# Optimization experiments

Measured on AMD Instinct MI355X. Metric: run time of the kernel, lower is better.

Reference implementation:

```python
import jax, jax.numpy as jnp
import numpy as np
import math
from jax import lax

ROT = math.radians(45.0)   # rotation_range in radians
TR = 1.0                   # translation_range
P = 50                     # n_particles
ITERS = 30                 # n_iterations
SUB = 256                  # fitness_subsample
MU = P // 2
C_SIGMA = 0.3
D_SIGMA = 1.0


def axis_angle_to_R(a):
    # a: [..., 3] -> [..., 3, 3] via Rodrigues' formula
    theta = jnp.linalg.norm(a, axis=-1, keepdims=True)
    axis = a / (theta + 1e-8)
    x, y, z = axis[..., 0], axis[..., 1], axis[..., 2]
    o = jnp.zeros_like(x)
    K = jnp.stack([jnp.stack([o, -z, y], -1),
                   jnp.stack([z, o, -x], -1),
                   jnp.stack([-y, x, o], -1)], -2)
    th = theta[..., None]
    I = jnp.eye(3, dtype=a.dtype)
    return I + jnp.sin(th) * K + (1.0 - jnp.cos(th)) * (K @ K)


def chamfer(x, y):
    # x: [M,S,3], y: [M,T,3] -> [M]; symmetric chamfer on squared NN distances
    d2 = (jnp.sum(x * x, -1)[:, :, None] + jnp.sum(y * y, -1)[:, None, :]
          - 2.0 * jnp.einsum('msd,mtd->mst', x, y))
    return jnp.min(d2, axis=2).mean(axis=1) + jnp.min(d2, axis=1).mean(axis=1)


def evaluate(src, tgt, positions):
    # src [B,S,3], tgt [B,T,3], positions [B,Pn,6] -> fitness [B,Pn]
    B, Pn, _ = positions.shape
    R = axis_angle_to_R(positions[..., :3])            # [B,Pn,3,3]
    t = positions[..., 3:]
    transformed = jnp.einsum('bnj,bpkj->bpnk', src, R) + t[:, :, None, :]
    x = transformed.reshape(B * Pn, -1, 3)
    y = jnp.broadcast_to(tgt[:, None], (B, Pn) + tgt.shape[1:]).reshape(B * Pn, -1, 3)
    return chamfer(x, y).reshape(B, Pn)


def clamp6(v):
    return jnp.concatenate([jnp.clip(v[..., :3], -ROT, ROT),
                            jnp.clip(v[..., 3:], -TR, TR)], axis=-1)


def run_cmaes(source, target, key):
    B, N, _ = source.shape
    M = target.shape[1]
    S = min(SUB, N)
    k1, k2, k3 = jax.random.split(key, 3)
    src = source[:, jax.random.permutation(k1, N)[:S], :] if S < N else source
    tgt = target[:, jax.random.permutation(k2, M)[:S], :] if S < M else target

    mean = jnp.zeros((B, 6), jnp.float32)
    sigma = jnp.concatenate([jnp.full((B, 3), ROT * 0.3, jnp.float32),
                             jnp.full((B, 3), TR * 0.3, jnp.float32)], axis=1)
    w = np.log(MU + 0.5) - np.log(np.arange(1, MU + 1))
    w = jnp.asarray(w / w.sum(), jnp.float32)       # [MU] recombination weights
    gbest_pos = mean
    gbest_fit = jnp.full((B,), jnp.inf, jnp.float32)

    def step(carry, k):
        mean, sigma, gbest_pos, gbest_fit = carry
        z = jax.random.normal(k, (B, P, 6), jnp.float32)
        off = clamp6(mean[:, None] + sigma[:, None] * z)        # [B,P,6]
        fit = evaluate(src, tgt, off)                            # [B,P]
        order = jnp.argsort(fit, axis=1)
        pidx = order[:, :MU]
        pz = jnp.take_along_axis(z, pidx[..., None], axis=1)     # [B,MU,6]
        ppos = jnp.take_along_axis(off, pidx[..., None], axis=1)
        mean_new = jnp.einsum('m,bmd->bd', w, ppos)
        mean_z = jnp.einsum('m,bmd->bd', w, pz)
        s = sigma * jnp.exp(C_SIGMA / D_SIGMA * (jnp.mean(jnp.abs(mean_z), -1, keepdims=True) - 1.0))
        s = jnp.concatenate([jnp.clip(s[:, :3], ROT * 0.01, ROT * 0.5),
                             jnp.clip(s[:, 3:], TR * 0.01, TR * 0.5)], axis=1)
        best_fit = jnp.take_along_axis(fit, order[:, :1], axis=1)[:, 0]
        best_pos = jnp.take_along_axis(off, order[:, :1, None], axis=1)[:, 0]
        impr = best_fit < gbest_fit
        gbest_pos = jnp.where(impr[:, None], best_pos, gbest_pos)
        gbest_fit = jnp.where(impr, best_fit, gbest_fit)
        return (mean_new, s, gbest_pos, gbest_fit), None

    keys = jax.random.split(k3, ITERS)
    (mean, sigma, gbest_pos, gbest_fit), _ = lax.scan(step, (mean, sigma, gbest_pos, gbest_fit), keys)

    mean_fit = evaluate(src, tgt, mean[:, None, :])[:, 0]
    gbest_pos = jnp.where((mean_fit < gbest_fit)[:, None], mean, gbest_pos)
    return gbest_pos


def _forward(source, target):
    # Optimization runs under no_grad in the original -> stop_gradient here
    gbest = lax.stop_gradient(run_cmaes(source, target, jax.random.key(42)))
    R = axis_angle_to_R(gbest[:, :3])          # [B,3,3]
    t = gbest[:, 3:]                            # [B,3]
    aligned = jnp.einsum('bnj,bkj->bnk', source, R) + t[:, None, :]
    return R, t, aligned


def setup_inputs() -> dict:
    key = jax.random.key(0)
    k1, k2 = jax.random.split(key)
    source = jax.random.normal(k1, (32, 16384, 3), jnp.float32)
    target = jax.random.normal(k2, (32, 16384, 3), jnp.float32)
    return {"source": source, "target": target}


def reference(source, target):
    return _forward(source, target)
```

## Files before the change

### kernel.cpp

```cpp
#include <hip/hip_runtime.h>
#include <stdint.h>
#include <math.h>

#define NB 32
#define NPTS 16384
#define SS 256
#define POPP 50
#define MUU 25
#define NITERS 30

#define ROTF  ((float)0.7853981633974483)
#define SIG0R ((float)(0.7853981633974483*0.3))
#define SIG0T ((float)0.3)
#define SLOR  ((float)(0.7853981633974483*0.01))
#define SHIR  ((float)(0.7853981633974483*0.5))
#define SLOT  ((float)0.01)
#define SHIT  ((float)0.5)
#define SQRT2F ((float)1.4142135623730951)
#define ULOW  (-0.99999994f)

__host__ __device__ inline uint32_t rotl32(uint32_t v, int n){ return (v<<n)|(v>>(32-n)); }

__host__ __device__ inline void tf2x32(uint32_t k0, uint32_t k1, uint32_t x0, uint32_t x1,
                                       uint32_t &o0, uint32_t &o1){
  uint32_t ks2 = k0 ^ k1 ^ 0x1BD11BDAu;
  x0 += k0; x1 += k1;
#define TFR(r) { x0 += x1; x1 = rotl32(x1, r); x1 ^= x0; }
  TFR(13) TFR(15) TFR(26) TFR(6)
  x0 += k1; x1 += ks2 + 1u;
  TFR(17) TFR(29) TFR(16) TFR(24)
  x0 += ks2; x1 += k0 + 2u;
  TFR(13) TFR(15) TFR(26) TFR(6)
  x0 += k0; x1 += k1 + 3u;
  TFR(17) TFR(29) TFR(16) TFR(24)
  x0 += k1; x1 += ks2 + 4u;
  TFR(13) TFR(15) TFR(26) TFR(6)
  x0 += ks2; x1 += k0 + 5u;
#undef TFR
  o0 = x0; o1 = x1;
}

__device__ inline float erfinv32(float x){
  float w = -log1pf(-x*x);
  float p;
  if (w < 5.0f) {
    w = w - 2.5f;
    p = 2.81022636e-08f;
    p = fmaf(p, w, 3.43273939e-07f);
    p = fmaf(p, w, -3.5233877e-06f);
    p = fmaf(p, w, -4.39150654e-06f);
    p = fmaf(p, w, 0.00021858087f);
    p = fmaf(p, w, -0.00125372503f);
    p = fmaf(p, w, -0.00417768164f);
    p = fmaf(p, w, 0.246640727f);
    p = fmaf(p, w, 1.50140941f);
  } else {
    w = sqrtf(w) - 3.0f;
    p = -0.000200214257f;
    p = fmaf(p, w, 0.000100950558f);
    p = fmaf(p, w, 0.00134934322f);
    p = fmaf(p, w, -0.00367342844f);
    p = fmaf(p, w, 0.00573950773f);
    p = fmaf(p, w, -0.0076224613f);
    p = fmaf(p, w, 0.00943887047f);
    p = fmaf(p, w, 1.00167406f);
    p = fmaf(p, w, 2.83297682f);
  }
  return p * x;
}

__device__ inline void axisangle_R(float ax, float ay, float az, float R[9]){
  float th = sqrtf(ax*ax + ay*ay + az*az);
  float den = th + 1e-8f;
  float ux = ax/den, uy = ay/den, uz = az/den;
  float s = sinf(th), c = cosf(th);
  float omc = 1.0f - c;
  float xx=ux*ux, yy=uy*uy, zz=uz*uz;
  float xy=ux*uy, xz=ux*uz, yz=uy*uz;
  R[0] = 1.0f + omc*(-(yy+zz));
  R[1] = s*(-uz) + omc*xy;
  R[2] = s*uy    + omc*xz;
  R[3] = s*uz    + omc*xy;
  R[4] = 1.0f + omc*(-(xx+zz));
  R[5] = s*(-ux) + omc*yz;
  R[6] = s*(-uy) + omc*xz;
  R[7] = s*ux    + omc*yz;
  R[8] = 1.0f + omc*(-(xx+yy));
}

struct WArr { float w[MUU]; };

__global__ void k_init(float* mean, float* sigma, float* gbest_pos, float* gbest_fit){
  int i = blockIdx.x*blockDim.x + threadIdx.x;
  if (i < NB*6){
    mean[i] = 0.0f;
    gbest_pos[i] = 0.0f;
    int d = i % 6;
    sigma[i] = (d < 3) ? SIG0R : SIG0T;
  }
  if (i < NB) gbest_fit[i] = INFINITY;
}

__global__ void k_genperm(uint64_t* comp, uint32_t sa0, uint32_t sa1,
                          uint32_t sb0, uint32_t sb1, int round){
  int i = blockIdx.x*blockDim.x + threadIdx.x;
  if (i >= 2*NPTS) return;
  int a = i >> 14;
  int idx = i & (NPTS-1);
  uint32_t kk0 = a ? sb0 : sa0;
  uint32_t kk1 = a ? sb1 : sa1;
  uint32_t o0,o1; tf2x32(kk0, kk1, 0u, (uint32_t)idx, o0, o1);
  uint32_t key = o0 ^ o1;
  uint64_t val = (round == 0) ? (uint64_t)idx : (comp[i] & 0x3FFFull);
  comp[i] = ((uint64_t)key << 28) | ((uint64_t)idx << 14) | val;
}

__global__ __launch_bounds__(1024) void k_sort_local(uint64_t* comp){
  __shared__ uint64_t buf[4096];
  int c = blockIdx.x;
  int base = c * 4096;
  int abase = (c & 3) * 4096;
  for (int t = threadIdx.x; t < 4096; t += 1024) buf[t] = comp[base + t];
  __syncthreads();
  for (int k = 2; k <= 4096; k <<= 1){
    for (int j = k >> 1; j > 0; j >>= 1){
      for (int idx = threadIdx.x; idx < 2048; idx += 1024){
        int i = ((idx & ~(j-1)) << 1) | (idx & (j-1));
        int pi = i | j;
        bool dir = (((abase + i) & k) == 0);
        uint64_t A = buf[i], Bv = buf[pi];
        bool sw = dir ? (A > Bv) : (A < Bv);
        if (sw){ buf[i] = Bv; buf[pi] = A; }
      }
      __syncthreads();
    }
  }
  for (int t = threadIdx.x; t < 4096; t += 1024) comp[base + t] = buf[t];
}

__global__ void k_sort_global(uint64_t* comp, int k, int j){
  int t = blockIdx.x*blockDim.x + threadIdx.x;
  if (t >= NPTS) return;
  int a = t >> 13;
  int idx = t & 8191;
  int i = ((idx & ~(j-1)) << 1) | (idx & (j-1));
  int pi = i | j;
  bool dir = ((i & k) == 0);
  uint64_t* arr = comp + (size_t)a * NPTS;
  uint64_t A = arr[i], Bv = arr[pi];
  bool sw = dir ? (A > Bv) : (A < Bv);
  if (sw){ arr[i] = Bv; arr[pi] = A; }
}

__global__ __launch_bounds__(1024) void k_sort_finish(uint64_t* comp, int k){
  __shared__ uint64_t buf[4096];
  int c = blockIdx.x;
  int base = c * 4096;
  int abase = (c & 3) * 4096;
  for (int t = threadIdx.x; t < 4096; t += 1024) buf[t] = comp[base + t];
  __syncthreads();
  for (int j = 2048; j > 0; j >>= 1){
    for (int idx = threadIdx.x; idx < 2048; idx += 1024){
      int i = ((idx & ~(j-1)) << 1) | (idx & (j-1));
      int pi = i | j;
      bool dir = (((abase + i) & k) == 0);
      uint64_t A = buf[i], Bv = buf[pi];
      bool sw = dir ? (A > Bv) : (A < Bv);
      if (sw){ buf[i] = Bv; buf[pi] = A; }
    }
    __syncthreads();
  }
  for (int t = threadIdx.x; t < 4096; t += 1024) comp[base + t] = buf[t];
}

__global__ void k_gather(const uint64_t* comp, const float* source, const float* target,
                         float* src_sub, float* tgt_sub){
  int t = blockIdx.x*blockDim.x + threadIdx.x;
  if (t >= 2*NB*SS) return;
  int a = t / (NB*SS);
  int r = t % (NB*SS);
  int b = r / SS;
  int s2 = r % SS;
  int val = (int)(comp[(size_t)a*NPTS + s2] & 0x3FFFull);
  const float* inp = a ? target : source;
  float* outp = a ? tgt_sub : src_sub;
  for (int d = 0; d < 3; ++d)
    outp[((size_t)b*SS + s2)*3 + d] = inp[((size_t)b*NPTS + val)*3 + d];
}

__global__ __launch_bounds__(128) void k_se(uint32_t ka, uint32_t kb,
    const float* __restrict__ mean, const float* __restrict__ sigma,
    const float* __restrict__ src_sub, const float* __restrict__ tgt_sub,
    float* __restrict__ z_buf, float* __restrict__ off_buf,
    float* __restrict__ fit){
  int c = blockIdx.x;
  int b = c / POPP;
  int tid = threadIdx.x;
  int wave = tid >> 6;
  int lane = tid & 63;
  __shared__ float qoff[6];
  __shared__ float4 ysd[SS];
  __shared__ float4 xsd[SS];
  __shared__ float wpart[2];

  if (tid < 6){
    int i = c*6 + tid;
    uint32_t o0,o1; tf2x32(ka, kb, 0u, (uint32_t)i, o0, o1);
    uint32_t bits = o0 ^ o1;
    float u = __uint_as_float((bits >> 9) | 0x3F800000u) - 1.0f;
    u = u * 2.0f + ULOW;
    u = fmaxf(ULOW, u);
    float zz = SQRT2F * erfinv32(u);
    float m = mean[b*6 + tid], sg = sigma[b*6 + tid];
    float v = fmaf(sg, zz, m);
    float lim = (tid < 3) ? ROTF : 1.0f;
    v = fminf(fmaxf(v, -lim), lim);
    z_buf[i] = zz; off_buf[i] = v; qoff[tid] = v;
  }
  __syncthreads();

  float R[9];
  axisangle_R(qoff[0], qoff[1], qoff[2], R);
  float tx=qoff[3], ty=qoff[4], tz=qoff[5];

  for (int i = tid; i < SS; i += 128){
    const float* tp = tgt_sub + ((size_t)b*SS + i)*3;
    float Y0=tp[0], Y1=tp[1], Y2=tp[2];
    float sy = fmaf(Y2,Y2, fmaf(Y1,Y1, Y0*Y0));
    ysd[i] = make_float4(-2.0f*Y0, -2.0f*Y1, -2.0f*Y2, sy);
  }

  int xi0 = wave*128 + lane;
  int xi1 = xi0 + 64;
  float px0,py0,pz0,sx0, px1,py1,pz1,sx1;
  {
    const float* sp = src_sub + ((size_t)b*SS + xi0)*3;
    float X0=sp[0], X1=sp[1], X2=sp[2];
    px0 = fmaf(X2, R[2], fmaf(X1, R[1], X0*R[0])) + tx;
    py0 = fmaf(X2, R[5], fmaf(X1, R[4], X0*R[3])) + ty;
    pz0 = fmaf(X2, R[8], fmaf(X1, R[7], X0*R[6])) + tz;
    sx0 = fmaf(pz0,pz0, fmaf(py0,py0, px0*px0));
    xsd[xi0] = make_float4(-2.0f*px0, -2.0f*py0, -2.0f*pz0, sx0);
  }
  {
    const float* sp = src_sub + ((size_t)b*SS + xi1)*3;
    float X0=sp[0], X1=sp[1], X2=sp[2];
    px1 = fmaf(X2, R[2], fmaf(X1, R[1], X0*R[0])) + tx;
    py1 = fmaf(X2, R[5], fmaf(X1, R[4], X0*R[3])) + ty;
    pz1 = fmaf(X2, R[8], fmaf(X1, R[7], X0*R[6])) + tz;
    sx1 = fmaf(pz1,pz1, fmaf(py1,py1, px1*px1));
    xsd[xi1] = make_float4(-2.0f*px1, -2.0f*py1, -2.0f*pz1, sx1);
  }
  __syncthreads();

  float rm0 = INFINITY, rm1 = INFINITY;
  #pragma unroll 8
  for (int t = 0; t < SS; ++t){
    float4 yv = ysd[t];
    rm0 = fminf(rm0, fmaf(px0, yv.x, fmaf(py0, yv.y, fmaf(pz0, yv.z, yv.w))));
    rm1 = fminf(rm1, fmaf(px1, yv.x, fmaf(py1, yv.y, fmaf(pz1, yv.z, yv.w))));
  }
  float acc = (sx0 + rm0) + (sx1 + rm1);

  float4 yv0 = ysd[xi0];
  float4 yv1 = ysd[xi1];
  float yx0 = -0.5f*yv0.x, yy0 = -0.5f*yv0.y, yz0 = -0.5f*yv0.z, sy0 = yv0.w;
  float yx1 = -0.5f*yv1.x, yy1 = -0.5f*yv1.y, yz1 = -0.5f*yv1.z, sy1 = yv1.w;
  float cm0 = INFINITY, cm1 = INFINITY;
  #pragma unroll 8
  for (int t = 0; t < SS; ++t){
    float4 xv = xsd[t];
    cm0 = fminf(cm0, fmaf(yx0, xv.x, fmaf(yy0, xv.y, fmaf(yz0, xv.z, xv.w))));
    cm1 = fminf(cm1, fmaf(yx1, xv.x, fmaf(yy1, xv.y, fmaf(yz1, xv.z, xv.w))));
  }
  acc += (sy0 + cm0) + (sy1 + cm1);

  for (int m = 32; m > 0; m >>= 1) acc += __shfl_xor(acc, m, 64);
  if (lane == 0) wpart[wave] = acc;
  __syncthreads();
  if (tid == 0) fit[c] = (wpart[0] + wpart[1]) * (1.0f/256.0f);
}

__global__ __launch_bounds__(128) void k_eval(const float* __restrict__ pos, int Pn,
    const float* __restrict__ src_sub, const float* __restrict__ tgt_sub,
    float* __restrict__ fit){
  int c = blockIdx.x;
  int b = c / Pn;
  int tid = threadIdx.x;
  int wave = tid >> 6;
  int lane = tid & 63;
  __shared__ float4 ysd[SS];
  __shared__ float4 xsd[SS];
  __shared__ float wpart[2];

  const float* q = pos + (size_t)c*6;
  float R[9];
  axisangle_R(q[0], q[1], q[2], R);
  float tx=q[3], ty=q[4], tz=q[5];

  for (int i = tid; i < SS; i += 128){
    const float* tp = tgt_sub + ((size_t)b*SS + i)*3;
    float Y0=tp[0], Y1=tp[1], Y2=tp[2];
    float sy = fmaf(Y2,Y2, fmaf(Y1,Y1, Y0*Y0));
    ysd[i] = make_float4(-2.0f*Y0, -2.0f*Y1, -2.0f*Y2, sy);
  }

  int xi0 = wave*128 + lane;
  int xi1 = xi0 + 64;
  float px0,py0,pz0,sx0, px1,py1,pz1,sx1;
  {
    const float* sp = src_sub + ((size_t)b*SS + xi0)*3;
    float X0=sp[0], X1=sp[1], X2=sp[2];
    px0 = fmaf(X2, R[2], fmaf(X1, R[1], X0*R[0])) + tx;
    py0 = fmaf(X2, R[5], fmaf(X1, R[4], X0*R[3])) + ty;
    pz0 = fmaf(X2, R[8], fmaf(X1, R[7], X0*R[6])) + tz;
    sx0 = fmaf(pz0,pz0, fmaf(py0,py0, px0*px0));
    xsd[xi0] = make_float4(-2.0f*px0, -2.0f*py0, -2.0f*pz0, sx0);
  }
  {
    const float* sp = src_sub + ((size_t)b*SS + xi1)*3;
    float X0=sp[0], X1=sp[1], X2=sp[2];
    px1 = fmaf(X2, R[2], fmaf(X1, R[1], X0*R[0])) + tx;
    py1 = fmaf(X2, R[5], fmaf(X1, R[4], X0*R[3])) + ty;
    pz1 = fmaf(X2, R[8], fmaf(X1, R[7], X0*R[6])) + tz;
    sx1 = fmaf(pz1,pz1, fmaf(py1,py1, px1*px1));
    xsd[xi1] = make_float4(-2.0f*px1, -2.0f*py1, -2.0f*pz1, sx1);
  }
  __syncthreads();

  float rm0 = INFINITY, rm1 = INFINITY;
  #pragma unroll 8
  for (int t = 0; t < SS; ++t){
    float4 yv = ysd[t];
    rm0 = fminf(rm0, fmaf(px0, yv.x, fmaf(py0, yv.y, fmaf(pz0, yv.z, yv.w))));
    rm1 = fminf(rm1, fmaf(px1, yv.x, fmaf(py1, yv.y, fmaf(pz1, yv.z, yv.w))));
  }
  float acc = (sx0 + rm0) + (sx1 + rm1);

  float4 yv0 = ysd[xi0];
  float4 yv1 = ysd[xi1];
  float yx0 = -0.5f*yv0.x, yy0 = -0.5f*yv0.y, yz0 = -0.5f*yv0.z, sy0 = yv0.w;
  float yx1 = -0.5f*yv1.x, yy1 = -0.5f*yv1.y, yz1 = -0.5f*yv1.z, sy1 = yv1.w;
  float cm0 = INFINITY, cm1 = INFINITY;
  #pragma unroll 8
  for (int t = 0; t < SS; ++t){
    float4 xv = xsd[t];
    cm0 = fminf(cm0, fmaf(yx0, xv.x, fmaf(yy0, xv.y, fmaf(yz0, xv.z, xv.w))));
    cm1 = fminf(cm1, fmaf(yx1, xv.x, fmaf(yy1, xv.y, fmaf(yz1, xv.z, xv.w))));
  }
  acc += (sy0 + cm0) + (sy1 + cm1);

  for (int m = 32; m > 0; m >>= 1) acc += __shfl_xor(acc, m, 64);
  if (lane == 0) wpart[wave] = acc;
  __syncthreads();
  if (tid == 0) fit[c] = (wpart[0] + wpart[1]) * (1.0f/256.0f);
}

__global__ __launch_bounds__(64) void k_update(const float* __restrict__ fit,
    const float* __restrict__ off, const float* __restrict__ z,
    float* mean, float* sigma, float* gbest_pos, float* gbest_fit, WArr W){
  int b = blockIdx.x;
  int tid = threadIdx.x;
  __shared__ float lfit[POPP];
  __shared__ int order[POPP];
  __shared__ float mn[6], mz[6];
  if (tid < POPP) lfit[tid] = fit[b*POPP + tid];
  __syncthreads();
  if (tid < POPP){
    float f = lfit[tid];
    int r = 0;
    for (int j = 0; j < POPP; ++j){
      float fj = lfit[j];
      r += (fj < f) || (fj == f && j < tid);
    }
    order[r] = tid;
  }
  __syncthreads();
  if (tid < 6){
    float a = 0.0f, bz = 0.0f;
    for (int m = 0; m < MUU; ++m){
      int idx = order[m];
      a  = fmaf(W.w[m], off[((size_t)b*POPP + idx)*6 + tid], a);
      bz = fmaf(W.w[m], z  [((size_t)b*POPP + idx)*6 + tid], bz);
    }
    mn[tid] = a; mz[tid] = bz;
  }
  __syncthreads();
  if (tid == 0){
    float avg = (((((fabsf(mz[0])+fabsf(mz[1]))+fabsf(mz[2]))+fabsf(mz[3]))+fabsf(mz[4]))+fabsf(mz[5])) / 6.0f;
    float e = expf(0.3f * (avg - 1.0f));
    for (int d = 0; d < 6; ++d){
      float sN = sigma[b*6 + d] * e;
      float lo = (d < 3) ? SLOR : SLOT;
      float hi = (d < 3) ? SHIR : SHIT;
      sN = fminf(fmaxf(sN, lo), hi);
      sigma[b*6 + d] = sN;
      mean[b*6 + d] = mn[d];
    }
    int i0 = order[0];
    float bf = lfit[i0];
    if (bf < gbest_fit[b]){
      gbest_fit[b] = bf;
      for (int d = 0; d < 6; ++d) gbest_pos[b*6 + d] = off[((size_t)b*POPP + i0)*6 + d];
    }
  }
}

__global__ void k_finalize(const float* mean, const float* mean_fit,
                           const float* gbest_pos, const float* gbest_fit, float* out){
  int b = blockIdx.x;
  if (threadIdx.x != 0) return;
  bool um = mean_fit[b] < gbest_fit[b];
  float g[6];
  for (int d = 0; d < 6; ++d) g[d] = um ? mean[b*6 + d] : gbest_pos[b*6 + d];
  float R[9];
  axisangle_R(g[0], g[1], g[2], R);
  for (int i = 0; i < 9; ++i) out[b*9 + i] = R[i];
  for (int d = 0; d < 3; ++d) out[NB*9 + b*3 + d] = g[3 + d];
}

__global__ void k_aligned(const float* __restrict__ src, const float* __restrict__ out_rt,
                          float* __restrict__ aligned){
  int idx = blockIdx.x*blockDim.x + threadIdx.x;
  if (idx >= NB*NPTS) return;
  int b = idx / NPTS;
  const float* R = out_rt + b*9;
  const float* t = out_rt + NB*9 + b*3;
  const float* p = src + (size_t)idx*3;
  float X0=p[0], X1=p[1], X2=p[2];
  float* o = aligned + (size_t)idx*3;
  o[0] = fmaf(X2, R[2], fmaf(X1, R[1], X0*R[0])) + t[0];
  o[1] = fmaf(X2, R[5], fmaf(X1, R[4], X0*R[3])) + t[1];
  o[2] = fmaf(X2, R[8], fmaf(X1, R[7], X0*R[6])) + t[2];
}

struct HKey { uint32_t a, b; };
static inline HKey h_tf(HKey k, uint32_t x0, uint32_t x1){
  uint32_t o0,o1; tf2x32(k.a, k.b, x0, x1, o0, o1);
  return {o0, o1};
}

static void run_sort(uint64_t* comp, hipStream_t stream){
  hipLaunchKernelGGL(k_sort_local,  dim3(8),  dim3(1024), 0, stream, comp);
  hipLaunchKernelGGL(k_sort_global, dim3(64), dim3(256),  0, stream, comp, 8192, 4096);
  hipLaunchKernelGGL(k_sort_finish, dim3(8),  dim3(1024), 0, stream, comp, 8192);
  hipLaunchKernelGGL(k_sort_global, dim3(64), dim3(256),  0, stream, comp, 16384, 8192);
  hipLaunchKernelGGL(k_sort_global, dim3(64), dim3(256),  0, stream, comp, 16384, 4096);
  hipLaunchKernelGGL(k_sort_finish, dim3(8),  dim3(1024), 0, stream, comp, 16384);
}

extern "C" void kernel_launch(void* const* d_in, const int* in_sizes, int n_in,
                              void* d_out, int out_size, void* d_ws, size_t ws_size,
                              hipStream_t stream){
  const float* source = (const float*)d_in[0];
  const float* target = (const float*)d_in[1];
  float* out = (float*)d_out;

  uint8_t* w = (uint8_t*)d_ws;
  size_t o = 0;
  auto alloc = [&](size_t bytes){ void* p = w + o; o += (bytes + 255) & ~(size_t)255; return p; };
  uint64_t* comp   = (uint64_t*)alloc(2*(size_t)NPTS*8);
  float* src_sub   = (float*)alloc((size_t)NB*SS*3*4);
  float* tgt_sub   = (float*)alloc((size_t)NB*SS*3*4);
  float* z_buf     = (float*)alloc((size_t)NB*POPP*6*4);
  float* off_buf   = (float*)alloc((size_t)NB*POPP*6*4);
  float* fit_buf   = (float*)alloc((size_t)NB*POPP*4);
  float* mean_buf  = (float*)alloc((size_t)NB*6*4);
  float* sigma_buf = (float*)alloc((size_t)NB*6*4);
  float* gb_pos    = (float*)alloc((size_t)NB*6*4);
  float* gb_fit    = (float*)alloc((size_t)NB*4);
  float* mean_fit  = (float*)alloc((size_t)NB*4);
  (void)ws_size; (void)in_sizes; (void)n_in; (void)out_size;

  HKey key0 = {0u, 42u};
  HKey k1 = h_tf(key0, 0u, 0u);
  HKey k2 = h_tf(key0, 0u, 1u);
  HKey k3 = h_tf(key0, 0u, 2u);
  HKey srcA  = h_tf(k1, 0u, 0u);
  HKey srcS1 = h_tf(k1, 0u, 1u);
  HKey srcS2 = h_tf(srcA, 0u, 1u);
  HKey tgtA  = h_tf(k2, 0u, 0u);
  HKey tgtS1 = h_tf(k2, 0u, 1u);
  HKey tgtS2 = h_tf(tgtA, 0u, 1u);
  HKey itk[NITERS];
  for (int j = 0; j < NITERS; ++j) itk[j] = h_tf(k3, 0u, (uint32_t)j);

  WArr W;
  {
    double lw[MUU], s = 0.0;
    for (int m = 0; m < MUU; ++m){ lw[m] = log((double)MUU + 0.5) - log((double)(m+1)); s += lw[m]; }
    for (int m = 0; m < MUU; ++m) W.w[m] = (float)(lw[m] / s);
  }

  hipLaunchKernelGGL(k_init, dim3(1), dim3(256), 0, stream, mean_buf, sigma_buf, gb_pos, gb_fit);

  hipLaunchKernelGGL(k_genperm, dim3(128), dim3(256), 0, stream,
                     comp, srcS1.a, srcS1.b, tgtS1.a, tgtS1.b, 0);
  run_sort(comp, stream);
  hipLaunchKernelGGL(k_genperm, dim3(128), dim3(256), 0, stream,
                     comp, srcS2.a, srcS2.b, tgtS2.a, tgtS2.b, 1);
  run_sort(comp, stream);
  hipLaunchKernelGGL(k_gather, dim3(64), dim3(256), 0, stream,
                     comp, source, target, src_sub, tgt_sub);

  for (int it = 0; it < NITERS; ++it){
    hipLaunchKernelGGL(k_se, dim3(NB*POPP), dim3(128), 0, stream,
                       itk[it].a, itk[it].b, mean_buf, sigma_buf,
                       src_sub, tgt_sub, z_buf, off_buf, fit_buf);
    hipLaunchKernelGGL(k_update, dim3(NB), dim3(64), 0, stream,
                       fit_buf, off_buf, z_buf, mean_buf, sigma_buf, gb_pos, gb_fit, W);
  }

  hipLaunchKernelGGL(k_eval, dim3(NB), dim3(128), 0, stream,
                     mean_buf, 1, src_sub, tgt_sub, mean_fit);
  hipLaunchKernelGGL(k_finalize, dim3(NB), dim3(64), 0, stream,
                     mean_buf, mean_fit, gb_pos, gb_fit, out);
  hipLaunchKernelGGL(k_aligned, dim3((NB*NPTS + 255)/256), dim3(256), 0, stream,
                     source, out, out + NB*9 + NB*3);
}
```

Before: 1.006 ms.

## Fuse chamfer row/col min loops with 4 points per lane and split t-range across waves

```diff
diff --git a/kernel.cpp b/kernel.cpp
--- a/kernel.cpp
+++ b/kernel.cpp
@@ -201,6 +201,8 @@
   __shared__ float qoff[6];
   __shared__ float4 ysd[SS];
   __shared__ float4 xsd[SS];
+  __shared__ float rmp[2][SS];
+  __shared__ float cmp[2][SS];
   __shared__ float wpart[2];
 
   if (tid < 6){
@@ -230,50 +232,67 @@
     ysd[i] = make_float4(-2.0f*Y0, -2.0f*Y1, -2.0f*Y2, sy);
   }
 
-  int xi0 = wave*128 + lane;
-  int xi1 = xi0 + 64;
-  float px0,py0,pz0,sx0, px1,py1,pz1,sx1;
-  {
-    const float* sp = src_sub + ((size_t)b*SS + xi0)*3;
+  #pragma unroll
+  for (int rep = 0; rep < 2; ++rep){
+    int xi = tid + rep*128;
+    const float* sp = src_sub + ((size_t)b*SS + xi)*3;
     float X0=sp[0], X1=sp[1], X2=sp[2];
-    px0 = fmaf(X2, R[2], fmaf(X1, R[1], X0*R[0])) + tx;
-    py0 = fmaf(X2, R[5], fmaf(X1, R[4], X0*R[3])) + ty;
-    pz0 = fmaf(X2, R[8], fmaf(X1, R[7], X0*R[6])) + tz;
-    sx0 = fmaf(pz0,pz0, fmaf(py0,py0, px0*px0));
-    xsd[xi0] = make_float4(-2.0f*px0, -2.0f*py0, -2.0f*pz0, sx0);
-  }
-  {
-    const float* sp = src_sub + ((size_t)b*SS + xi1)*3;
-    float X0=sp[0], X1=sp[1], X2=sp[2];
-    px1 = fmaf(X2, R[2], fmaf(X1, R[1], X0*R[0])) + tx;
-    py1 = fmaf(X2, R[5], fmaf(X1, R[4], X0*R[3])) + ty;
-    pz1 = fmaf(X2, R[8], fmaf(X1, R[7], X0*R[6])) + tz;
-    sx1 = fmaf(pz1,pz1, fmaf(py1,py1, px1*px1));
-    xsd[xi1] = make_float4(-2.0f*px1, -2.0f*py1, -2.0f*pz1, sx1);
-  }
-  __syncthreads();
-
-  float rm0 = INFINITY, rm1 = INFINITY;
+    float px = fmaf(X2, R[2], fmaf(X1, R[1], X0*R[0])) + tx;
+    float py = fmaf(X2, R[5], fmaf(X1, R[4], X0*R[3])) + ty;
+    float pz = fmaf(X2, R[8], fmaf(X1, R[7], X0*R[6])) + tz;
+    float sx = fmaf(pz,pz, fmaf(py,py, px*px));
+    xsd[xi] = make_float4(-2.0f*px, -2.0f*py, -2.0f*pz, sx);
+  }
+  __syncthreads();
+
+  float pxj[4],pyj[4],pzj[4],sxj[4];
+  float yxj[4],yyj[4],yzj[4],syj[4];
+  #pragma unroll
+  for (int j = 0; j < 4; ++j){
+    int i = lane + 64*j;
+    float4 xv = xsd[i];
+    pxj[j] = -0.5f*xv.x; pyj[j] = -0.5f*xv.y; pzj[j] = -0.5f*xv.z; sxj[j] = xv.w;
+    float4 yv = ysd[i];
+    yxj[j] = -0.5f*yv.x; yyj[j] = -0.5f*yv.y; yzj[j] = -0.5f*yv.z; syj[j] = yv.w;
+  }
+
+  float rm0=INFINITY, rm1=INFINITY, rm2=INFINITY, rm3=INFINITY;
+  float cm0=INFINITY, cm1=INFINITY, cm2=INFINITY, cm3=INFINITY;
+  int tbeg = wave*128;
   #pragma unroll 8
-  for (int t = 0; t < SS; ++t){
+  for (int t = tbeg; t < tbeg+128; ++t){
     float4 yv = ysd[t];
-    rm0 = fminf(rm0, fmaf(px0, yv.x, fmaf(py0, yv.y, fmaf(pz0, yv.z, yv.w))));
-    rm1 = fminf(rm1, fmaf(px1, yv.x, fmaf(py1, yv.y, fmaf(pz1, yv.z, yv.w))));
-  }
-  float acc = (sx0 + rm0) + (sx1 + rm1);
-
-  float4 yv0 = ysd[xi0];
-  float4 yv1 = ysd[xi1];
-  float yx0 = -0.5f*yv0.x, yy0 = -0.5f*yv0.y, yz0 = -0.5f*yv0.z, sy0 = yv0.w;
-  float yx1 = -0.5f*yv1.x, yy1 = -0.5f*yv1.y, yz1 = -0.5f*yv1.z, sy1 = yv1.w;
-  float cm0 = INFINITY, cm1 = INFINITY;
-  #pragma unroll 8
-  for (int t = 0; t < SS; ++t){
     float4 xv = xsd[t];
-    cm0 = fminf(cm0, fmaf(yx0, xv.x, fmaf(yy0, xv.y, fmaf(yz0, xv.z, xv.w))));
-    cm1 = fminf(cm1, fmaf(yx1, xv.x, fmaf(yy1, xv.y, fmaf(yz1, xv.z, xv.w))));
-  }
-  acc += (sy0 + cm0) + (sy1 + cm1);
+    rm0 = fminf(rm0, fmaf(pxj[0], yv.x, fmaf(pyj[0], yv.y, fmaf(pzj[0], yv.z, yv.w))));
+    rm1 = fminf(rm1, fmaf(pxj[1], yv.x, fmaf(pyj[1], yv.y, fmaf(pzj[1], yv.z, yv.w))));
+    rm2 = fminf(rm2, fmaf(pxj[2], yv.x, fmaf(pyj[2], yv.y, fmaf(pzj[2], yv.z, yv.w))));
+    rm3 = fminf(rm3, fmaf(pxj[3], yv.x, fmaf(pyj[3], yv.y, fmaf(pzj[3], yv.z, yv.w))));
+    cm0 = fminf(cm0, fmaf(yxj[0], xv.x, fmaf(yyj[0], xv.y, fmaf(yzj[0], xv.z, xv.w))));
+    cm1 = fminf(cm1, fmaf(yxj[1], xv.x, fmaf(yyj[1], xv.y, fmaf(yzj[1], xv.z, xv.w))));
+    cm2 = fminf(cm2, fmaf(yxj[2], xv.x, fmaf(yyj[2], xv.y, fmaf(yzj[2], xv.z, xv.w))));
+    cm3 = fminf(cm3, fmaf(yxj[3], xv.x, fmaf(yyj[3], xv.y, fmaf(yzj[3], xv.z, xv.w))));
+  }
+
+  rmp[wave][lane+  0] = rm0;  cmp[wave][lane+  0] = cm0;
+  rmp[wave][lane+ 64] = rm1;  cmp[wave][lane+ 64] = cm1;
+  rmp[wave][lane+128] = rm2;  cmp[wave][lane+128] = cm2;
+  rmp[wave][lane+192] = rm3;  cmp[wave][lane+192] = cm3;
+  __syncthreads();
+
+  float acc;
+  if (wave == 0){
+    float f0 = sxj[0] + fminf(rmp[0][lane+  0], rmp[1][lane+  0]);
+    float f1 = sxj[1] + fminf(rmp[0][lane+ 64], rmp[1][lane+ 64]);
+    float f2 = sxj[2] + fminf(rmp[0][lane+128], rmp[1][lane+128]);
+    float f3 = sxj[3] + fminf(rmp[0][lane+192], rmp[1][lane+192]);
+    acc = (f0 + f1) + (f2 + f3);
+  } else {
+    float f0 = syj[0] + fminf(cmp[0][lane+  0], cmp[1][lane+  0]);
+    float f1 = syj[1] + fminf(cmp[0][lane+ 64], cmp[1][lane+ 64]);
+    float f2 = syj[2] + fminf(cmp[0][lane+128], cmp[1][lane+128]);
+    float f3 = syj[3] + fminf(cmp[0][lane+192], cmp[1][lane+192]);
+    acc = (f0 + f1) + (f2 + f3);
+  }
 
   for (int m = 32; m > 0; m >>= 1) acc += __shfl_xor(acc, m, 64);
   if (lane == 0) wpart[wave] = acc;
```

New measurement: 1.017 ms. No clear change (+1.1%).
